# Performance work log

Hardware: AMD Instinct MI355X
Metric: run time of the kernel (lower is better)

The kernel has to match this reference:

```python
import jax, jax.numpy as jnp
import numpy as np

NB_HEAD = 16

def setup_inputs() -> dict:
    key = jax.random.key(0)
    ks = jax.random.split(key, 5)
    B, S, E = 2, 2048, 1024
    sc = 1.0 / np.sqrt(E)
    x = jax.random.normal(ks[0], (B, S, E), dtype=jnp.float32)
    Wq = jax.random.normal(ks[1], (E, E), dtype=jnp.float32) * sc
    Wk = jax.random.normal(ks[2], (E, E), dtype=jnp.float32) * sc
    Wv = jax.random.normal(ks[3], (E, E), dtype=jnp.float32) * sc
    Wo = jax.random.normal(ks[4], (E, E), dtype=jnp.float32) * sc
    z = jnp.zeros((E,), dtype=jnp.float32)
    return {"x": x, "Wq": Wq, "bq": z, "Wk": Wk, "bk": z, "Wv": Wv, "bv": z, "Wo": Wo, "bo": z}

def reference(x, Wq, bq, Wk, bk, Wv, bv, Wo, bo):
    B, S, E = x.shape
    H = NB_HEAD
    D = E // H
    # projections -> [B, S, H, D]
    q = (x @ Wq + bq).reshape(B, S, H, D)
    k = (x @ Wk + bk).reshape(B, S, H, D)
    v = (x @ Wv + bv).reshape(B, S, H, D)
    # NOTE: original scales by sqrt(embedding_size), not sqrt(head_dim)
    scores = jnp.einsum('bqhd,bkhd->bhqk', q, k) / jnp.sqrt(jnp.float32(E))
    causal = jnp.tril(jnp.ones((S, S), dtype=bool))  # mask=True path
    scores = jnp.where(causal[None, None], scores, -jnp.inf)
    p = jax.nn.softmax(scores, axis=-1)
    attn = jnp.einsum('bhqk,bkhd->bqhd', p, v).reshape(B, S, E)
    return attn @ Wo + bo
```

## Files before the change

kernel.cpp:

```cpp
#include <hip/hip_runtime.h>
#include <hip/hip_bf16.h>

#define S_LEN 2048
#define EMB   1024
#define NHEAD 16
#define HDIM  64
#define NBATCH 2
#define M_ROWS (NBATCH * S_LEN)

typedef __attribute__((ext_vector_type(8))) __bf16 bf16x8;
typedef __attribute__((ext_vector_type(8))) short short8;
typedef __attribute__((ext_vector_type(4))) short short4_t;
typedef __attribute__((ext_vector_type(4))) float floatx4;

__device__ inline bf16x8 load_frag(const short* p) {
    short8 v = *(const short8*)p;
    return __builtin_bit_cast(bf16x8, v);
}
__device__ inline floatx4 mfma16(bf16x8 a, bf16x8 b, floatx4 c) {
    return __builtin_amdgcn_mfma_f32_16x16x32_bf16(a, b, c, 0, 0, 0);
}
__device__ inline short f2bf_bits(float f) {
    return __builtin_bit_cast(short, __float2bfloat16(f));
}

#if defined(__has_builtin)
#if __has_builtin(__builtin_amdgcn_global_load_lds)
#define HAVE_ASYNC_LDS 1
#endif
#endif

#ifdef HAVE_ASYNC_LDS
typedef __attribute__((address_space(1))) const void glb_void;
typedef __attribute__((address_space(3))) void lds_void;
__device__ __forceinline__ void load16_to_lds(const void* g, void* l) {
    __builtin_amdgcn_global_load_lds((glb_void*)g, (lds_void*)l, 16, 0, 0);
}
#endif

__global__ __launch_bounds__(256) void prep_kernel(
        const float* __restrict__ x, short* __restrict__ xb,
        const float* __restrict__ w0, const float* __restrict__ w1,
        const float* __restrict__ w2, const float* __restrict__ w3,
        short* __restrict__ o0, short* __restrict__ o1,
        short* __restrict__ o2, short* __restrict__ o3) {
    const int t = threadIdx.x;
    if (blockIdx.x < 2048) {
        int idx = (blockIdx.x * 256 + t) * 8;
        float4 a = *(const float4*)&x[idx];
        float4 b = *(const float4*)&x[idx + 4];
        short8 o;
        o[0] = f2bf_bits(a.x); o[1] = f2bf_bits(a.y);
        o[2] = f2bf_bits(a.z); o[3] = f2bf_bits(a.w);
        o[4] = f2bf_bits(b.x); o[5] = f2bf_bits(b.y);
        o[6] = f2bf_bits(b.z); o[7] = f2bf_bits(b.w);
        *(short8*)&xb[idx] = o;
    } else {
        __shared__ float tile[32][33];
        int tb = blockIdx.x - 2048;
        int z = tb >> 10, rem = tb & 1023;
        int bx = rem & 31, by = rem >> 5;
        const float* in; short* out;
        switch (z) {
            case 0: in = w0; out = o0; break;
            case 1: in = w1; out = o1; break;
            case 2: in = w2; out = o2; break;
            default: in = w3; out = o3; break;
        }
        int tx = t & 31, ty = t >> 5;
        int c = bx * 32 + tx;
        int r0 = by * 32;
#pragma unroll
        for (int i = 0; i < 4; i++) {
            int r = r0 + ty + i * 8;
            tile[ty + i * 8][tx] = in[(size_t)r * EMB + c];
        }
        __syncthreads();
        int rr = r0 + tx;
        int cc0 = bx * 32;
#pragma unroll
        for (int i = 0; i < 4; i++) {
            int cc = cc0 + ty + i * 8;
            out[(size_t)cc * EMB + rr] = f2bf_bits(tile[tx][ty + i * 8]);
        }
    }
}

__global__ __launch_bounds__(256, 2) void qkv_fused(
        const short* __restrict__ x,
        const short* __restrict__ WqT, const short* __restrict__ WkT,
        const short* __restrict__ WvT,
        const float* __restrict__ pbq, const float* __restrict__ pbk,
        const float* __restrict__ pbv,
        short* __restrict__ Q, short* __restrict__ K, short* __restrict__ Vt) {
    __shared__ short lds_a[128 * 64];
    __shared__ short lds_b[3][64 * 64];

    const int t = threadIdx.x;
    const int wave = t >> 6, lane = t & 63;
    const int wm = wave >> 1, wn = wave & 1;
    const int l15 = lane & 15, quad = lane >> 4;
    const int rowA0 = blockIdx.x * 128;
    const int colB0 = blockIdx.y * 64;

    const short* Bts[3] = {WqT, WkT, WvT};

    floatx4 acc[3][4][2] = {};

    for (int k0 = 0; k0 < EMB; k0 += 64) {
#pragma unroll
        for (int i = 0; i < 4; i++) {
            int idx = i * 256 + t;
            int row = idx >> 3;
            int cg = ((idx & 7) ^ (row & 7)) * 8;
            const short* ga = &x[(size_t)(rowA0 + row) * EMB + k0 + cg];
#ifdef HAVE_ASYNC_LDS
            load16_to_lds(ga, &lds_a[(i * 256 + wave * 64) * 8]);
#else
            *(short8*)&lds_a[idx * 8] = *(const short8*)ga;
#endif
        }
#pragma unroll
        for (int m = 0; m < 3; m++)
#pragma unroll
            for (int i = 0; i < 2; i++) {
                int idx = i * 256 + t;
                int row = idx >> 3;
                int cg = ((idx & 7) ^ (row & 7)) * 8;
                const short* gb = &Bts[m][(size_t)(colB0 + row) * EMB + k0 + cg];
#ifdef HAVE_ASYNC_LDS
                load16_to_lds(gb, &lds_b[m][(i * 256 + wave * 64) * 8]);
#else
                *(short8*)&lds_b[m][idx * 8] = *(const short8*)gb;
#endif
            }
        __syncthreads();
#pragma unroll
        for (int kk = 0; kk < 2; kk++) {
            bf16x8 af[4];
#pragma unroll
            for (int i = 0; i < 4; i++)
                af[i] = load_frag(&lds_a[(wm * 64 + i * 16 + l15) * 64 +
                                         (((kk * 4 + quad) ^ (l15 & 7)) * 8)]);
#pragma unroll
            for (int m = 0; m < 3; m++)
#pragma unroll
                for (int j = 0; j < 2; j++) {
                    bf16x8 bfr = load_frag(
                        &lds_b[m][(wn * 32 + j * 16 + l15) * 64 +
                                  (((kk * 4 + quad) ^ (l15 & 7)) * 8)]);
#pragma unroll
                    for (int i = 0; i < 4; i++)
                        acc[m][i][j] = mfma16(af[i], bfr, acc[m][i][j]);
                }
        }
        __syncthreads();
    }

#pragma unroll
    for (int i = 0; i < 4; i++)
#pragma unroll
        for (int j = 0; j < 2; j++) {
            int col = colB0 + wn * 32 + j * 16 + l15;
            int h = col >> 6, d = col & 63;
            int row0 = rowA0 + wm * 64 + i * 16 + quad * 4;
            int b = row0 >> 11, s0 = row0 & 2047;
            float bvq = pbq[col], bvk = pbk[col], bvv = pbv[col];
#pragma unroll
            for (int r = 0; r < 4; r++)
                Q[((size_t)((b * NHEAD + h) * S_LEN + s0 + r)) * HDIM + d] =
                    f2bf_bits(acc[0][i][j][r] + bvq);
#pragma unroll
            for (int r = 0; r < 4; r++)
                K[((size_t)((b * NHEAD + h) * S_LEN + s0 + r)) * HDIM + d] =
                    f2bf_bits(acc[1][i][j][r] + bvk);
            short4_t pack;
#pragma unroll
            for (int r = 0; r < 4; r++)
                pack[r] = f2bf_bits(acc[2][i][j][r] + bvv);
            *(short4_t*)&Vt[((size_t)((b * NHEAD + h) * HDIM + d)) * S_LEN + s0] = pack;
        }
}

__global__ __launch_bounds__(256) void out_gemm(
        const short* __restrict__ A, const short* __restrict__ Bt,
        const float* __restrict__ bias, float* __restrict__ Cout) {
    __shared__ short lds_a[128 * 64];
    __shared__ short lds_b[64 * 64];

    const int t = threadIdx.x;
    const int wave = t >> 6, lane = t & 63;
    const int wm = wave >> 1, wn = wave & 1;
    const int l15 = lane & 15, quad = lane >> 4;
    const int rowA0 = blockIdx.x * 128;
    const int rowB0 = blockIdx.y * 64;

    floatx4 acc[4][2] = {};

    for (int k0 = 0; k0 < EMB; k0 += 64) {
#pragma unroll
        for (int i = 0; i < 4; i++) {
            int idx = i * 256 + t;
            int row = idx >> 3;
            int cg = ((idx & 7) ^ (row & 7)) * 8;
            const short* ga = &A[(size_t)(rowA0 + row) * EMB + k0 + cg];
#ifdef HAVE_ASYNC_LDS
            load16_to_lds(ga, &lds_a[(i * 256 + wave * 64) * 8]);
#else
            *(short8*)&lds_a[idx * 8] = *(const short8*)ga;
#endif
        }
#pragma unroll
        for (int i = 0; i < 2; i++) {
            int idx = i * 256 + t;
            int row = idx >> 3;
            int cg = ((idx & 7) ^ (row & 7)) * 8;
            const short* gb = &Bt[(size_t)(rowB0 + row) * EMB + k0 + cg];
#ifdef HAVE_ASYNC_LDS
            load16_to_lds(gb, &lds_b[(i * 256 + wave * 64) * 8]);
#else
            *(short8*)&lds_b[idx * 8] = *(const short8*)gb;
#endif
        }
        __syncthreads();
#pragma unroll
        for (int kk = 0; kk < 2; kk++) {
            bf16x8 af[4], bfr[2];
#pragma unroll
            for (int i = 0; i < 4; i++)
                af[i] = load_frag(&lds_a[(wm * 64 + i * 16 + l15) * 64 +
                                         (((kk * 4 + quad) ^ (l15 & 7)) * 8)]);
#pragma unroll
            for (int j = 0; j < 2; j++)
                bfr[j] = load_frag(&lds_b[(wn * 32 + j * 16 + l15) * 64 +
                                          (((kk * 4 + quad) ^ (l15 & 7)) * 8)]);
#pragma unroll
            for (int i = 0; i < 4; i++)
#pragma unroll
                for (int j = 0; j < 2; j++)
                    acc[i][j] = mfma16(af[i], bfr[j], acc[i][j]);
        }
        __syncthreads();
    }

#pragma unroll
    for (int i = 0; i < 4; i++)
#pragma unroll
        for (int j = 0; j < 2; j++) {
            int col = rowB0 + wn * 32 + j * 16 + l15;
            float bv = bias[col];
            int row0 = rowA0 + wm * 64 + i * 16 + quad * 4;
#pragma unroll
            for (int r = 0; r < 4; r++)
                Cout[(size_t)(row0 + r) * EMB + col] = acc[i][j][r] + bv;
        }
}

__global__ __launch_bounds__(256) void attn_kernel(
        const short* __restrict__ Q, const short* __restrict__ K,
        const short* __restrict__ Vt, short* __restrict__ O) {
    constexpr int LDPP = 136;
    __shared__ short lds_k[128 * 64];
    __shared__ short lds_v[64 * 128];
    __shared__ short lds_p[4][32 * LDPP];

    const int t = threadIdx.x;
    const int wave = t >> 6, lane = t & 63;
    const int l15 = lane & 15, quad = lane >> 4;
    const int bh = blockIdx.x;
    const int slot = blockIdx.y;
    const short* Qh = Q + (size_t)bh * S_LEN * HDIM;
    const short* Kh = K + (size_t)bh * S_LEN * HDIM;
    const short* Vh = Vt + (size_t)bh * HDIM * S_LEN;
    const int b = bh >> 4, h = bh & 15;

    const float C1 = 0.03125f * 1.44269504088896f;
    const float M  = 12.0f;

    const int tile = wave >> 1, wsub = wave & 1;
    const int qt = tile == 0 ? (31 - slot) : slot;
    const int q0 = qt * 64;
    const int qbase = q0 + wsub * 32;
    const int nch_this = (qt + 2) >> 1;
    const int nch_total = (33 - slot) >> 1;

    bf16x8 ones;
    {
        short8 o1v;
        short one = f2bf_bits(1.0f);
#pragma unroll
        for (int i = 0; i < 8; i++) o1v[i] = one;
        ones = __builtin_bit_cast(bf16x8, o1v);
    }

    bf16x8 qf[2][2];
#pragma unroll
    for (int st = 0; st < 2; st++) {
        int qrow = qbase + st * 16 + l15;
        qf[st][0] = load_frag(&Qh[(size_t)qrow * HDIM + quad * 8]);
        qf[st][1] = load_frag(&Qh[(size_t)qrow * HDIM + 32 + quad * 8]);
    }

    floatx4 accO[2][4] = {};
    floatx4 accL[2] = {};

#pragma unroll 1
    for (int cd = 0; cd < nch_total; cd++) {
        const int kv0 = cd * 128;
#pragma unroll
        for (int i = 0; i < 4; i++) {
            int idx = i * 256 + t;
            int krow = idx >> 3, kcl = idx & 7;
            int kcg = kcl ^ (krow & 7);
            int vrow = idx >> 4, vcl = idx & 15;
            int vcg = vcl ^ (vrow & 15);
            const short* gk = &Kh[(size_t)(kv0 + krow) * HDIM + kcg * 8];
            const short* gv = &Vh[(size_t)vrow * S_LEN + kv0 + vcg * 8];
#ifdef HAVE_ASYNC_LDS
            int base = (i * 256 + wave * 64) * 8;
            load16_to_lds(gk, &lds_k[base]);
            load16_to_lds(gv, &lds_v[base]);
#else
            *(short8*)&lds_k[idx * 8] = *(const short8*)gk;
            *(short8*)&lds_v[idx * 8] = *(const short8*)gv;
#endif
        }
        __syncthreads();

        if (cd < nch_this) {
            if (kv0 + 128 > qbase) {
#pragma unroll
                for (int c = 0; c < 8; c++) {
                    int krow = c * 16 + l15;
                    bf16x8 kf0 = load_frag(&lds_k[krow * 64 + (quad ^ (l15 & 7)) * 8]);
                    bf16x8 kf1 = load_frag(&lds_k[krow * 64 + ((4 + quad) ^ (l15 & 7)) * 8]);
#pragma unroll
                    for (int st = 0; st < 2; st++) {
                        floatx4 z = {};
                        z = mfma16(qf[st][0], kf0, z);
                        floatx4 s = mfma16(qf[st][1], kf1, z);
#pragma unroll
                        for (int r = 0; r < 4; r++) {
                            int qrow = qbase + st * 16 + quad * 4 + r;
                            int kcol = kv0 + c * 16 + l15;
                            float p = __builtin_amdgcn_exp2f(
                                __builtin_fmaf(s[r], C1, -M));
                            p = (kcol > qrow) ? 0.f : p;
                            lds_p[wave][(st * 16 + quad * 4 + r) * LDPP +
                                        c * 16 + l15] = f2bf_bits(p);
                        }
                    }
                }
            } else {
#pragma unroll
                for (int c = 0; c < 8; c++) {
                    int krow = c * 16 + l15;
                    bf16x8 kf0 = load_frag(&lds_k[krow * 64 + (quad ^ (l15 & 7)) * 8]);
                    bf16x8 kf1 = load_frag(&lds_k[krow * 64 + ((4 + quad) ^ (l15 & 7)) * 8]);
#pragma unroll
                    for (int st = 0; st < 2; st++) {
                        floatx4 z = {};
                        z = mfma16(qf[st][0], kf0, z);
                        floatx4 s = mfma16(qf[st][1], kf1, z);
#pragma unroll
                        for (int r = 0; r < 4; r++) {
                            float p = __builtin_amdgcn_exp2f(
                                __builtin_fmaf(s[r], C1, -M));
                            lds_p[wave][(st * 16 + quad * 4 + r) * LDPP +
                                        c * 16 + l15] = f2bf_bits(p);
                        }
                    }
                }
            }

#pragma unroll
            for (int ks = 0; ks < 4; ks++) {
                bf16x8 pf0 = load_frag(&lds_p[wave][l15 * LDPP + ks * 32 + quad * 8]);
                bf16x8 pf1 = load_frag(&lds_p[wave][(16 + l15) * LDPP + ks * 32 + quad * 8]);
                accL[0] = mfma16(pf0, ones, accL[0]);
                accL[1] = mfma16(pf1, ones, accL[1]);
#pragma unroll
                for (int dt = 0; dt < 4; dt++) {
                    int vrow = dt * 16 + l15;
                    bf16x8 vf = load_frag(
                        &lds_v[vrow * 128 + ((ks * 4 + quad) ^ l15) * 8]);
                    accO[0][dt] = mfma16(pf0, vf, accO[0][dt]);
                    accO[1][dt] = mfma16(pf1, vf, accO[1][dt]);
                }
            }
        }
        __syncthreads();
    }

#pragma unroll
    for (int st = 0; st < 2; st++)
#pragma unroll
        for (int r = 0; r < 4; r++) {
            float inv = 1.0f / accL[st][r];
            int q = qbase + st * 16 + quad * 4 + r;
#pragma unroll
            for (int dt = 0; dt < 4; dt++) {
                int d = dt * 16 + l15;
                O[((size_t)(b * S_LEN + q) * NHEAD + h) * HDIM + d] =
                    f2bf_bits(accO[st][dt][r] * inv);
            }
        }
}

extern "C" void kernel_launch(void* const* d_in, const int* in_sizes, int n_in,
                              void* d_out, int out_size, void* d_ws, size_t ws_size,
                              hipStream_t stream) {
    const float* x  = (const float*)d_in[0];
    const float* Wq = (const float*)d_in[1];
    const float* bq = (const float*)d_in[2];
    const float* Wk = (const float*)d_in[3];
    const float* bk = (const float*)d_in[4];
    const float* Wv = (const float*)d_in[5];
    const float* bv = (const float*)d_in[6];
    const float* Wo = (const float*)d_in[7];
    const float* bo = (const float*)d_in[8];

    short* ws = (short*)d_ws;
    const size_t WSZ = (size_t)EMB * EMB;
    const size_t TSZ = (size_t)M_ROWS * EMB;
    short* xb  = ws;
    short* WqT = xb + TSZ;
    short* WkT = WqT + WSZ;
    short* WvT = WkT + WSZ;
    short* WoT = WvT + WSZ;
    short* Qb  = WoT + WSZ;
    short* Kb  = Qb + TSZ;
    short* Vtb = Kb + TSZ;
    short* Ab  = Vtb + TSZ;

    prep_kernel<<<dim3(2048 + 4096), 256, 0, stream>>>(
        x, xb, Wq, Wk, Wv, Wo, WqT, WkT, WvT, WoT);

    qkv_fused<<<dim3(M_ROWS / 128, EMB / 64), 256, 0, stream>>>(
        xb, WqT, WkT, WvT, bq, bk, bv, Qb, Kb, Vtb);

    attn_kernel<<<dim3(NBATCH * NHEAD, 16), 256, 0, stream>>>(Qb, Kb, Vtb, Ab);

    out_gemm<<<dim3(M_ROWS / 128, EMB / 64), 256, 0, stream>>>(
        Ab, WoT, bo, (float*)d_out);
}
```

Measured before the change: 178.0 us.

## Give each wave rows from both paired query tiles to balance causal work

Before, waves 0-1 of a block handled the high (long) query tile and waves 2-3 the low (short) one, so the low-tile waves sat idle in later KV chunks. Now every wave owns 16 rows of the high tile and 16 rows of the low tile. It computes the low-tile part only while that tile is still active, and applies the causal mask per subtile when the chunk touches the diagonal. This spreads MFMA work evenly across the four waves, at the cost of extra branches and predicated MFMA inside the inner loops.

```diff
diff --git a/kernel.cpp b/kernel.cpp
--- a/kernel.cpp
+++ b/kernel.cpp
@@ -277,12 +277,11 @@
     const float C1 = 0.03125f * 1.44269504088896f;
     const float M  = 12.0f;
 
-    const int tile = wave >> 1, wsub = wave & 1;
-    const int qt = tile == 0 ? (31 - slot) : slot;
-    const int q0 = qt * 64;
-    const int qbase = q0 + wsub * 32;
-    const int nch_this = (qt + 2) >> 1;
-    const int nch_total = (33 - slot) >> 1;
+    const int qtH = 31 - slot, qtL = slot;
+    const int qbH = qtH * 64 + wave * 16;
+    const int qbL = qtL * 64 + wave * 16;
+    const int nchH = (qtH + 2) >> 1;
+    const int nchL = (qtL + 2) >> 1;
 
     bf16x8 ones;
     {
@@ -294,19 +293,18 @@
     }
 
     bf16x8 qf[2][2];
-#pragma unroll
-    for (int st = 0; st < 2; st++) {
-        int qrow = qbase + st * 16 + l15;
-        qf[st][0] = load_frag(&Qh[(size_t)qrow * HDIM + quad * 8]);
-        qf[st][1] = load_frag(&Qh[(size_t)qrow * HDIM + 32 + quad * 8]);
-    }
+    qf[0][0] = load_frag(&Qh[(size_t)(qbH + l15) * HDIM + quad * 8]);
+    qf[0][1] = load_frag(&Qh[(size_t)(qbH + l15) * HDIM + 32 + quad * 8]);
+    qf[1][0] = load_frag(&Qh[(size_t)(qbL + l15) * HDIM + quad * 8]);
+    qf[1][1] = load_frag(&Qh[(size_t)(qbL + l15) * HDIM + 32 + quad * 8]);
 
     floatx4 accO[2][4] = {};
     floatx4 accL[2] = {};
 
 #pragma unroll 1
-    for (int cd = 0; cd < nch_total; cd++) {
+    for (int cd = 0; cd < nchH; cd++) {
         const int kv0 = cd * 128;
+        const bool actL = (cd < nchL);
 #pragma unroll
         for (int i = 0; i < 4; i++) {
             int idx = i * 256 + t;
@@ -327,77 +325,77 @@
         }
         __syncthreads();
 
-        if (cd < nch_this) {
-            if (kv0 + 128 > qbase) {
-#pragma unroll
-                for (int c = 0; c < 8; c++) {
-                    int krow = c * 16 + l15;
-                    bf16x8 kf0 = load_frag(&lds_k[krow * 64 + (quad ^ (l15 & 7)) * 8]);
-                    bf16x8 kf1 = load_frag(&lds_k[krow * 64 + ((4 + quad) ^ (l15 & 7)) * 8]);
-#pragma unroll
-                    for (int st = 0; st < 2; st++) {
-                        floatx4 z = {};
-                        z = mfma16(qf[st][0], kf0, z);
-                        floatx4 s = mfma16(qf[st][1], kf1, z);
-#pragma unroll
-                        for (int r = 0; r < 4; r++) {
-                            int qrow = qbase + st * 16 + quad * 4 + r;
-                            int kcol = kv0 + c * 16 + l15;
-                            float p = __builtin_amdgcn_exp2f(
-                                __builtin_fmaf(s[r], C1, -M));
-                            p = (kcol > qrow) ? 0.f : p;
-                            lds_p[wave][(st * 16 + quad * 4 + r) * LDPP +
-                                        c * 16 + l15] = f2bf_bits(p);
-                        }
+        const bool diagH = (kv0 + 128 > qbH);
+        const bool diagL = (kv0 + 128 > qbL);
+#pragma unroll
+        for (int c = 0; c < 8; c++) {
+            int krow = c * 16 + l15;
+            bf16x8 kf0 = load_frag(&lds_k[krow * 64 + (quad ^ (l15 & 7)) * 8]);
+            bf16x8 kf1 = load_frag(&lds_k[krow * 64 + ((4 + quad) ^ (l15 & 7)) * 8]);
+            {
+                floatx4 z = {};
+                z = mfma16(qf[0][0], kf0, z);
+                floatx4 s = mfma16(qf[0][1], kf1, z);
+#pragma unroll
+                for (int r = 0; r < 4; r++) {
+                    float p = __builtin_amdgcn_exp2f(
+                        __builtin_fmaf(s[r], C1, -M));
+                    if (diagH) {
+                        int qrow = qbH + quad * 4 + r;
+                        int kcol = kv0 + c * 16 + l15;
+                        p = (kcol > qrow) ? 0.f : p;
                     }
+                    lds_p[wave][(quad * 4 + r) * LDPP + c * 16 + l15] =
+                        f2bf_bits(p);
                 }
-            } else {
-#pragma unroll
-                for (int c = 0; c < 8; c++) {
-                    int krow = c * 16 + l15;
-                    bf16x8 kf0 = load_frag(&lds_k[krow * 64 + (quad ^ (l15 & 7)) * 8]);
-                    bf16x8 kf1 = load_frag(&lds_k[krow * 64 + ((4 + quad) ^ (l15 & 7)) * 8]);
-#pragma unroll
-                    for (int st = 0; st < 2; st++) {
-                        floatx4 z = {};
-                        z = mfma16(qf[st][0], kf0, z);
-                        floatx4 s = mfma16(qf[st][1], kf1, z);
-#pragma unroll
-                        for (int r = 0; r < 4; r++) {
-                            float p = __builtin_amdgcn_exp2f(
-                                __builtin_fmaf(s[r], C1, -M));
-                            lds_p[wave][(st * 16 + quad * 4 + r) * LDPP +
-                                        c * 16 + l15] = f2bf_bits(p);
-                        }
+            }
+            if (actL) {
+                floatx4 z = {};
+                z = mfma16(qf[1][0], kf0, z);
+                floatx4 s = mfma16(qf[1][1], kf1, z);
+#pragma unroll
+                for (int r = 0; r < 4; r++) {
+                    float p = __builtin_amdgcn_exp2f(
+                        __builtin_fmaf(s[r], C1, -M));
+                    if (diagL) {
+                        int qrow = qbL + quad * 4 + r;
+                        int kcol = kv0 + c * 16 + l15;
+                        p = (kcol > qrow) ? 0.f : p;
                     }
+                    lds_p[wave][(16 + quad * 4 + r) * LDPP + c * 16 + l15] =
+                        f2bf_bits(p);
                 }
             }
-
-#pragma unroll
-            for (int ks = 0; ks < 4; ks++) {
-                bf16x8 pf0 = load_frag(&lds_p[wave][l15 * LDPP + ks * 32 + quad * 8]);
-                bf16x8 pf1 = load_frag(&lds_p[wave][(16 + l15) * LDPP + ks * 32 + quad * 8]);
-                accL[0] = mfma16(pf0, ones, accL[0]);
+        }
+
+#pragma unroll
+        for (int ks = 0; ks < 4; ks++) {
+            bf16x8 pf0 = load_frag(&lds_p[wave][l15 * LDPP + ks * 32 + quad * 8]);
+            accL[0] = mfma16(pf0, ones, accL[0]);
+            bf16x8 pf1;
+            if (actL) {
+                pf1 = load_frag(&lds_p[wave][(16 + l15) * LDPP + ks * 32 + quad * 8]);
                 accL[1] = mfma16(pf1, ones, accL[1]);
-#pragma unroll
-                for (int dt = 0; dt < 4; dt++) {
-                    int vrow = dt * 16 + l15;
-                    bf16x8 vf = load_frag(
-                        &lds_v[vrow * 128 + ((ks * 4 + quad) ^ l15) * 8]);
-                    accO[0][dt] = mfma16(pf0, vf, accO[0][dt]);
-                    accO[1][dt] = mfma16(pf1, vf, accO[1][dt]);
-                }
-            }
-        }
-        __syncthreads();
-    }
-
-#pragma unroll
-    for (int st = 0; st < 2; st++)
+            }
+#pragma unroll
+            for (int dt = 0; dt < 4; dt++) {
+                int vrow = dt * 16 + l15;
+                bf16x8 vf = load_frag(
+                    &lds_v[vrow * 128 + ((ks * 4 + quad) ^ l15) * 8]);
+                accO[0][dt] = mfma16(pf0, vf, accO[0][dt]);
+                if (actL) accO[1][dt] = mfma16(pf1, vf, accO[1][dt]);
+            }
+        }
+        __syncthreads();
+    }
+
+#pragma unroll
+    for (int st = 0; st < 2; st++) {
+        int qb = st == 0 ? qbH : qbL;
 #pragma unroll
         for (int r = 0; r < 4; r++) {
             float inv = 1.0f / accL[st][r];
-            int q = qbase + st * 16 + quad * 4 + r;
+            int q = qb + quad * 4 + r;
 #pragma unroll
             for (int dt = 0; dt < 4; dt++) {
                 int d = dt * 16 + l15;
@@ -405,6 +403,7 @@
                     f2bf_bits(accO[st][dt][r] * inv);
             }
         }
+    }
 }
 
 extern "C" void kernel_launch(void* const* d_in, const int* in_sizes, int n_in,
```

Measured after the change: 180.0 us. No clear change (+1.1%).

## Restructure attention blocks to 128-query tiles with 64-key chunks

Applied to the files above, without the earlier changes.

Replaces the paired light/heavy 64-row query tiles (load balancing via slot pairing) with one 128-row query tile per block, ordered heaviest first, and streams K/V in 64-key chunks instead of 128. LDS shrinks to 64x64 tiles, the padded P buffer becomes an XOR-swizzled layout, and the masked and unmasked score paths merge into one loop with a diagonal flag. This cuts LDS footprint and wasted masked work per chunk and may raise occupancy. In exchange it doubles the number of barriers per key range and loses the explicit pairing-based load balance across blocks.

```diff
diff --git a/kernel.cpp b/kernel.cpp
--- a/kernel.cpp
+++ b/kernel.cpp
@@ -259,16 +259,19 @@
 __global__ __launch_bounds__(256) void attn_kernel(
         const short* __restrict__ Q, const short* __restrict__ K,
         const short* __restrict__ Vt, short* __restrict__ O) {
-    constexpr int LDPP = 136;
-    __shared__ short lds_k[128 * 64];
-    __shared__ short lds_v[64 * 128];
-    __shared__ short lds_p[4][32 * LDPP];
+    __shared__ short lds_k[64 * 64];
+    __shared__ short lds_v[64 * 64];
+    __shared__ short lds_p[4][32 * 64];
 
     const int t = threadIdx.x;
     const int wave = t >> 6, lane = t & 63;
     const int l15 = lane & 15, quad = lane >> 4;
     const int bh = blockIdx.x;
-    const int slot = blockIdx.y;
+    const int qt = 15 - blockIdx.y;
+    const int q0 = qt * 128;
+    const int nch = 2 * qt + 2;
+    const int qbase = q0 + wave * 32;
+    const int myNch = 2 * qt + 1 + (wave >> 1);
     const short* Qh = Q + (size_t)bh * S_LEN * HDIM;
     const short* Kh = K + (size_t)bh * S_LEN * HDIM;
     const short* Vh = Vt + (size_t)bh * HDIM * S_LEN;
@@ -277,13 +280,6 @@
     const float C1 = 0.03125f * 1.44269504088896f;
     const float M  = 12.0f;
 
-    const int tile = wave >> 1, wsub = wave & 1;
-    const int qt = tile == 0 ? (31 - slot) : slot;
-    const int q0 = qt * 64;
-    const int qbase = q0 + wsub * 32;
-    const int nch_this = (qt + 2) >> 1;
-    const int nch_total = (33 - slot) >> 1;
-
     bf16x8 ones;
     {
         short8 o1v;
@@ -305,17 +301,15 @@
     floatx4 accL[2] = {};
 
 #pragma unroll 1
-    for (int cd = 0; cd < nch_total; cd++) {
-        const int kv0 = cd * 128;
-#pragma unroll
-        for (int i = 0; i < 4; i++) {
+    for (int cd = 0; cd < nch; cd++) {
+        const int kv0 = cd * 64;
+#pragma unroll
+        for (int i = 0; i < 2; i++) {
             int idx = i * 256 + t;
-            int krow = idx >> 3, kcl = idx & 7;
-            int kcg = kcl ^ (krow & 7);
-            int vrow = idx >> 4, vcl = idx & 15;
-            int vcg = vcl ^ (vrow & 15);
-            const short* gk = &Kh[(size_t)(kv0 + krow) * HDIM + kcg * 8];
-            const short* gv = &Vh[(size_t)vrow * S_LEN + kv0 + vcg * 8];
+            int row = idx >> 3, cl = idx & 7;
+            int cg = (cl ^ (row & 7)) * 8;
+            const short* gk = &Kh[(size_t)(kv0 + row) * HDIM + cg];
+            const short* gv = &Vh[(size_t)row * S_LEN + kv0 + cg];
 #ifdef HAVE_ASYNC_LDS
             int base = (i * 256 + wave * 64) * 8;
             load16_to_lds(gk, &lds_k[base]);
@@ -327,63 +321,45 @@
         }
         __syncthreads();
 
-        if (cd < nch_this) {
-            if (kv0 + 128 > qbase) {
-#pragma unroll
-                for (int c = 0; c < 8; c++) {
-                    int krow = c * 16 + l15;
-                    bf16x8 kf0 = load_frag(&lds_k[krow * 64 + (quad ^ (l15 & 7)) * 8]);
-                    bf16x8 kf1 = load_frag(&lds_k[krow * 64 + ((4 + quad) ^ (l15 & 7)) * 8]);
-#pragma unroll
-                    for (int st = 0; st < 2; st++) {
-                        floatx4 z = {};
-                        z = mfma16(qf[st][0], kf0, z);
-                        floatx4 s = mfma16(qf[st][1], kf1, z);
-#pragma unroll
-                        for (int r = 0; r < 4; r++) {
+        if (cd < myNch) {
+            const bool diag = (kv0 + 64 > qbase);
+#pragma unroll
+            for (int c = 0; c < 4; c++) {
+                int krow = c * 16 + l15;
+                bf16x8 kf0 = load_frag(&lds_k[krow * 64 + (quad ^ (l15 & 7)) * 8]);
+                bf16x8 kf1 = load_frag(&lds_k[krow * 64 + ((4 + quad) ^ (l15 & 7)) * 8]);
+#pragma unroll
+                for (int st = 0; st < 2; st++) {
+                    floatx4 z = {};
+                    z = mfma16(qf[st][0], kf0, z);
+                    floatx4 s = mfma16(qf[st][1], kf1, z);
+#pragma unroll
+                    for (int r = 0; r < 4; r++) {
+                        float p = __builtin_amdgcn_exp2f(
+                            __builtin_fmaf(s[r], C1, -M));
+                        if (diag) {
                             int qrow = qbase + st * 16 + quad * 4 + r;
                             int kcol = kv0 + c * 16 + l15;
-                            float p = __builtin_amdgcn_exp2f(
-                                __builtin_fmaf(s[r], C1, -M));
                             p = (kcol > qrow) ? 0.f : p;
-                            lds_p[wave][(st * 16 + quad * 4 + r) * LDPP +
-                                        c * 16 + l15] = f2bf_bits(p);
                         }
-                    }
-                }
-            } else {
-#pragma unroll
-                for (int c = 0; c < 8; c++) {
-                    int krow = c * 16 + l15;
-                    bf16x8 kf0 = load_frag(&lds_k[krow * 64 + (quad ^ (l15 & 7)) * 8]);
-                    bf16x8 kf1 = load_frag(&lds_k[krow * 64 + ((4 + quad) ^ (l15 & 7)) * 8]);
-#pragma unroll
-                    for (int st = 0; st < 2; st++) {
-                        floatx4 z = {};
-                        z = mfma16(qf[st][0], kf0, z);
-                        floatx4 s = mfma16(qf[st][1], kf1, z);
-#pragma unroll
-                        for (int r = 0; r < 4; r++) {
-                            float p = __builtin_amdgcn_exp2f(
-                                __builtin_fmaf(s[r], C1, -M));
-                            lds_p[wave][(st * 16 + quad * 4 + r) * LDPP +
-                                        c * 16 + l15] = f2bf_bits(p);
-                        }
+                        int prow = st * 16 + quad * 4 + r;
+                        int swc = (c * 2 + (l15 >> 3)) ^ (prow & 7);
+                        lds_p[wave][prow * 64 + swc * 8 + (l15 & 7)] =
+                            f2bf_bits(p);
                     }
                 }
             }
-
-#pragma unroll
-            for (int ks = 0; ks < 4; ks++) {
-                bf16x8 pf0 = load_frag(&lds_p[wave][l15 * LDPP + ks * 32 + quad * 8]);
-                bf16x8 pf1 = load_frag(&lds_p[wave][(16 + l15) * LDPP + ks * 32 + quad * 8]);
+#pragma unroll
+            for (int ks = 0; ks < 2; ks++) {
+                int pc = ((ks * 4 + quad) ^ (l15 & 7)) * 8;
+                bf16x8 pf0 = load_frag(&lds_p[wave][l15 * 64 + pc]);
+                bf16x8 pf1 = load_frag(&lds_p[wave][(16 + l15) * 64 + pc]);
                 accL[0] = mfma16(pf0, ones, accL[0]);
                 accL[1] = mfma16(pf1, ones, accL[1]);
 #pragma unroll
                 for (int dt = 0; dt < 4; dt++) {
-                    int vrow = dt * 16 + l15;
                     bf16x8 vf = load_frag(
-                        &lds_v[vrow * 128 + ((ks * 4 + quad) ^ l15) * 8]);
+                        &lds_v[(dt * 16 + l15) * 64 + pc]);
                     accO[0][dt] = mfma16(pf0, vf, accO[0][dt]);
                     accO[1][dt] = mfma16(pf1, vf, accO[1][dt]);
                 }
@@ -439,7 +415,8 @@
     qkv_fused<<<dim3(M_ROWS / 128, EMB / 64), 256, 0, stream>>>(
         xb, WqT, WkT, WvT, bq, bk, bv, Qb, Kb, Vtb);
 
-    attn_kernel<<<dim3(NBATCH * NHEAD, 16), 256, 0, stream>>>(Qb, Kb, Vtb, Ab);
+    attn_kernel<<<dim3(NBATCH * NHEAD, S_LEN / 128), 256, 0, stream>>>(
+        Qb, Kb, Vtb, Ab);
 
     out_gemm<<<dim3(M_ROWS / 128, EMB / 64), 256, 0, stream>>>(
         Ab, WoT, bo, (float*)d_out);
```

Result: slower. 190.1 us (+6.8%).
